# Optimization experiments

Measured on AMD Instinct MI355X. Metric: run time of the kernel, lower is better.

The kernel has to match this reference:

```python
import jax, jax.numpy as jnp
import numpy as np

VOCAB = 50257
HID = 1024
MAXLEN = 64


def setup_inputs() -> dict:
    key = jax.random.key(0)
    ks = jax.random.split(key, 12)
    s = 1.0 / np.sqrt(HID)
    return {
        "input": jax.random.randint(ks[0], (1,), 0, VOCAB),
        "hidden": jax.random.normal(ks[1], (1, 1, HID), jnp.float32),
        "enc_outputs": jax.random.normal(ks[2], (MAXLEN, HID), jnp.float32),
        "emb": jax.random.normal(ks[3], (VOCAB, HID), jnp.float32),
        "attn_W": jax.random.uniform(ks[4], (MAXLEN, 2 * HID), jnp.float32, -s, s),
        "attn_b": jnp.zeros((MAXLEN,), jnp.float32),
        "comb_W": jax.random.uniform(ks[5], (HID, 2 * HID), jnp.float32, -s, s),
        "comb_b": jnp.zeros((HID,), jnp.float32),
        "gru_Wih": jax.random.uniform(ks[6], (3 * HID, HID), jnp.float32, -s, s),
        "gru_Whh": jax.random.uniform(ks[7], (3 * HID, HID), jnp.float32, -s, s),
        "gru_bih": jnp.zeros((3 * HID,), jnp.float32),
        "gru_bhh": jnp.zeros((3 * HID,), jnp.float32),
        "out_W": jax.random.uniform(ks[8], (VOCAB, HID), jnp.float32, -s, s),
        "out_b": jnp.zeros((VOCAB,), jnp.float32),
    }


def reference(input, hidden, enc_outputs, emb, attn_W, attn_b, comb_W, comb_b,
              gru_Wih, gru_Whh, gru_bih, gru_bhh, out_W, out_b):
    # embedded: [1, HID] (dropout is identity in eval / p=0)
    embedded = emb[input[0]][None, :]
    h = hidden[0]  # [1, HID]
    # attention over encoder positions
    cat_eh = jnp.concatenate([embedded, h], axis=1)           # [1, 2H]
    attn_weights = jax.nn.softmax(cat_eh @ attn_W.T + attn_b, axis=1)  # [1, MAXLEN]
    attn_applied = attn_weights @ enc_outputs                  # [1, HID]
    # combine
    x = jnp.concatenate([embedded, attn_applied], axis=1)      # [1, 2H]
    x = jax.nn.relu(x @ comb_W.T + comb_b)                     # [1, HID]
    # single GRU step (PyTorch gate order: r, z, n)
    gi = x @ gru_Wih.T + gru_bih                                # [1, 3H]
    gh = h @ gru_Whh.T + gru_bhh                                # [1, 3H]
    i_r, i_z, i_n = jnp.split(gi, 3, axis=1)
    h_r, h_z, h_n = jnp.split(gh, 3, axis=1)
    r = jax.nn.sigmoid(i_r + h_r)
    z = jax.nn.sigmoid(i_z + h_z)
    n = jnp.tanh(i_n + r * h_n)
    h_new = (1.0 - z) * n + z * h                               # [1, HID]
    # output projection + log-softmax
    logp = jax.nn.log_softmax(h_new @ out_W.T + out_b, axis=1)  # [1, VOCAB]
    return logp, h_new[None, :, :], attn_weights
```

## Files before the change

kernel.cpp:

```cpp
#include <hip/hip_runtime.h>
#include <hip/hip_bf16.h>

#define VOCAB 50257
#define HID   1024
#define MAXLEN 64

__device__ __forceinline__ float dot4(float4 a, float4 b){
  return a.x*b.x + a.y*b.y + a.z*b.z + a.w*b.w;
}
__device__ __forceinline__ float dot4f(float4 a, const float* v){
  return a.x*v[0] + a.y*v[1] + a.z*v[2] + a.w*v[3];
}

__global__ __launch_bounds__(256) void k_attn_scores(
    const int* tok_p, const float* hidden, const float* emb,
    const float* attn_W, const float* attn_b, float* ws_scores){
  int b = blockIdx.x, t = threadIdx.x;
  int tok = min(max(tok_p[0], 0), VOCAB-1);
  const float4* wv = (const float4*)(attn_W + (size_t)b*2048);
  const float4* ef = (const float4*)(emb + (size_t)tok*HID);
  const float4* hf = (const float4*)hidden;
  float acc = dot4(wv[t], ef[t]) + dot4(wv[256+t], hf[t]);
  #pragma unroll
  for (int k=32;k>=1;k>>=1) acc += __shfl_xor(acc,k);
  __shared__ float red[4];
  if ((t&63)==0) red[t>>6] = acc;
  __syncthreads();
  if (t==0) ws_scores[b] = red[0]+red[1]+red[2]+red[3] + attn_b[b];
}

__global__ __launch_bounds__(256) void k_combine_fused(
    const int* tok_p, const float* ws_scores, const float* enc,
    const float* emb, const float* comb_W, const float* comb_b,
    float* ws_x, float* out_attn){
  int t = threadIdx.x, wave = t>>6, lane = t&63;
  __shared__ float sw[MAXLEN];
  __shared__ float sa[HID];
  float s = ws_scores[lane];
  float m = s;
  #pragma unroll
  for (int k=32;k>=1;k>>=1) m = fmaxf(m, __shfl_xor(m,k));
  float e = expf(s-m), d = e;
  #pragma unroll
  for (int k=32;k>=1;k>>=1) d += __shfl_xor(d,k);
  float w = e/d;
  if (wave==0) sw[lane] = w;
  if (blockIdx.x==0 && wave==0) out_attn[lane] = w;
  __syncthreads();
  float4 a4 = make_float4(0.f,0.f,0.f,0.f);
  #pragma unroll 8
  for (int p=0;p<MAXLEN;p++){
    float wp = sw[p];
    float4 ev = *(const float4*)(enc + (size_t)p*HID + t*4);
    a4.x += wp*ev.x; a4.y += wp*ev.y; a4.z += wp*ev.z; a4.w += wp*ev.w;
  }
  *(float4*)(sa + t*4) = a4;
  __syncthreads();
  int row = blockIdx.x*4 + wave;
  int tok = min(max(tok_p[0], 0), VOCAB-1);
  const float4* wrow = (const float4*)(comb_W + (size_t)row*2048);
  const float4* erow = (const float4*)(emb + (size_t)tok*HID);
  const float4* av   = (const float4*)sa;
  float acc = 0.f;
  #pragma unroll
  for (int c=0;c<4;c++) acc += dot4(wrow[c*64+lane],     erow[c*64+lane]);
  #pragma unroll
  for (int c=0;c<4;c++) acc += dot4(wrow[256+c*64+lane], av[c*64+lane]);
  #pragma unroll
  for (int k=32;k>=1;k>>=1) acc += __shfl_xor(acc,k);
  if (lane==0) ws_x[row] = fmaxf(acc + comb_b[row], 0.f);
}

__global__ __launch_bounds__(256) void k_gru_fused(
    const float* ws_x, const float* hidden,
    const float* Wih, const float* Whh,
    const float* bih, const float* bhh,
    float* ws_h, float* out_h){
  int t = threadIdx.x, wave = t>>6, lane = t&63;
  __shared__ float part[2][6];
  for (int idx = wave; idx < 12; idx += 4){
    int u  = (idx >= 6) ? 1 : 0;
    int g  = idx - u*6;
    int hi = blockIdx.x*2 + u;
    bool ih = (g < 3);
    int gg = ih ? g : g-3;
    const float*  W = ih ? Wih : Whh;
    const float*  b = ih ? bih : bhh;
    const float4* vec  = ih ? (const float4*)ws_x : (const float4*)hidden;
    const float4* wrow = (const float4*)(W + ((size_t)gg*HID + hi)*HID);
    float acc = 0.f;
    #pragma unroll
    for (int c=0;c<4;c++) acc += dot4(wrow[c*64+lane], vec[c*64+lane]);
    #pragma unroll
    for (int k=32;k>=1;k>>=1) acc += __shfl_xor(acc,k);
    if (lane==0) part[u][g] = acc + b[gg*HID + hi];
  }
  __syncthreads();
  if (t < 2){
    int hi = blockIdx.x*2 + t;
    float r = 1.f/(1.f+expf(-(part[t][0] + part[t][3])));
    float z = 1.f/(1.f+expf(-(part[t][1] + part[t][4])));
    float n = tanhf(part[t][2] + r*part[t][5]);
    float h = hidden[hi];
    float hn = (1.f-z)*n + z*h;
    ws_h[hi]  = hn;
    out_h[hi] = hn;
  }
}

__global__ __launch_bounds__(256) void k_logits(
    const float* wsh, const float* out_W, const float* out_b,
    float* out_logits, float* ws_stats){
  int wave = threadIdx.x>>6, lane = threadIdx.x&63;
  int gw = blockIdx.x*4 + wave;
  float hv[16];
  #pragma unroll
  for (int c=0;c<4;c++)
    #pragma unroll
    for (int j=0;j<4;j++) hv[c*4+j] = wsh[c*256 + lane*4 + j];
  float m = -INFINITY, s = 0.f;
  for (int row = gw; row < VOCAB; row += 8192) {
    const float4* wrow = (const float4*)(out_W + (size_t)row*HID);
    float acc = 0.f;
    #pragma unroll
    for (int c=0;c<4;c++) acc += dot4f(wrow[c*64+lane], hv + c*4);
    #pragma unroll
    for (int k=32;k>=1;k>>=1) acc += __shfl_xor(acc,k);
    if (lane==0) {
      float logit = acc + out_b[row];
      out_logits[row] = logit;
      if (logit > m) { s = s*expf(m-logit) + 1.f; m = logit; }
      else s += expf(logit-m);
    }
  }
  __shared__ float sm[4], ss[4];
  if (lane==0){ sm[wave]=m; ss[wave]=s; }
  __syncthreads();
  if (threadIdx.x==0) {
    float M = fmaxf(fmaxf(sm[0],sm[1]),fmaxf(sm[2],sm[3]));
    float S = ss[0]*expf(sm[0]-M)+ss[1]*expf(sm[1]-M)
            + ss[2]*expf(sm[2]-M)+ss[3]*expf(sm[3]-M);
    ws_stats[blockIdx.x*2]   = M;
    ws_stats[blockIdx.x*2+1] = S;
  }
}

__global__ __launch_bounds__(256) void k_logp_fused(
    const float* ws_stats, float* out_logits){
  int t = threadIdx.x;
  float m = -INFINITY, s = 0.f;
  #pragma unroll
  for (int i=t;i<2048;i+=256){
    float mi = ws_stats[2*i], si = ws_stats[2*i+1];
    float M = fmaxf(m,mi);
    s = s*expf(m-M) + si*expf(mi-M);
    m = M;
  }
  #pragma unroll
  for (int k=32;k>=1;k>>=1){
    float mo = __shfl_xor(m,k), so = __shfl_xor(s,k);
    float M = fmaxf(m,mo);
    s = s*expf(m-M) + so*expf(mo-M);
    m = M;
  }
  __shared__ float sm[4], ss[4];
  __shared__ float slse;
  if ((t&63)==0){ sm[t>>6]=m; ss[t>>6]=s; }
  __syncthreads();
  if (t==0){
    float M = fmaxf(fmaxf(sm[0],sm[1]),fmaxf(sm[2],sm[3]));
    float S = ss[0]*expf(sm[0]-M)+ss[1]*expf(sm[1]-M)
            + ss[2]*expf(sm[2]-M)+ss[3]*expf(sm[3]-M);
    slse = M + logf(S);
  }
  __syncthreads();
  int i = blockIdx.x*256 + t;
  if (i < VOCAB) out_logits[i] -= slse;
}

extern "C" void kernel_launch(void* const* d_in, const int* in_sizes, int n_in,
                              void* d_out, int out_size, void* d_ws, size_t ws_size,
                              hipStream_t stream) {
  const int*   tok    = (const int*)d_in[0];
  const float* hidden = (const float*)d_in[1];
  const float* enc    = (const float*)d_in[2];
  const float* emb    = (const float*)d_in[3];
  const float* attn_W = (const float*)d_in[4];
  const float* attn_b = (const float*)d_in[5];
  const float* comb_W = (const float*)d_in[6];
  const float* comb_b = (const float*)d_in[7];
  const float* Wih    = (const float*)d_in[8];
  const float* Whh    = (const float*)d_in[9];
  const float* bih    = (const float*)d_in[10];
  const float* bhh    = (const float*)d_in[11];
  const float* out_W  = (const float*)d_in[12];
  const float* out_b  = (const float*)d_in[13];

  float* out      = (float*)d_out;
  float* out_logp = out;
  float* out_h    = out + VOCAB;
  float* out_attn = out + VOCAB + HID;

  float* ws        = (float*)d_ws;
  float* ws_scores = ws;
  float* ws_x      = ws + 128;
  float* ws_h      = ws + 1280;
  float* ws_stats  = ws + 2432;

  k_attn_scores  <<<64,   256, 0, stream>>>(tok, hidden, emb, attn_W, attn_b, ws_scores);
  k_combine_fused<<<256,  256, 0, stream>>>(tok, ws_scores, enc, emb, comb_W, comb_b, ws_x, out_attn);
  k_gru_fused    <<<512,  256, 0, stream>>>(ws_x, hidden, Wih, Whh, bih, bhh, ws_h, out_h);
  k_logits       <<<2048, 256, 0, stream>>>(ws_h, out_W, out_b, out_logp, ws_stats);
  k_logp_fused   <<<197,  256, 0, stream>>>(ws_stats, out_logp);
}
```

Baseline: 422.9 us.

## Fuse attention scores into combine kernel and reshape GRU kernel to one unit per block

Each combine block now computes all 64 attention scores itself, dropping the separate score kernel and one launch. The cost is that 256 blocks each redundantly read the full attn_W (512 KB), though this should mostly be served from cache. The GRU kernel now launches 1024 blocks of 6 waves, one wave per gate row, instead of 512 blocks that each looped over 12 rows. That gives more parallelism and removes the loop.

```diff
diff --git a/kernel.cpp b/kernel.cpp
--- a/kernel.cpp
+++ b/kernel.cpp
@@ -12,31 +12,32 @@
   return a.x*v[0] + a.y*v[1] + a.z*v[2] + a.w*v[3];
 }
 
-__global__ __launch_bounds__(256) void k_attn_scores(
-    const int* tok_p, const float* hidden, const float* emb,
-    const float* attn_W, const float* attn_b, float* ws_scores){
-  int b = blockIdx.x, t = threadIdx.x;
-  int tok = min(max(tok_p[0], 0), VOCAB-1);
-  const float4* wv = (const float4*)(attn_W + (size_t)b*2048);
-  const float4* ef = (const float4*)(emb + (size_t)tok*HID);
-  const float4* hf = (const float4*)hidden;
-  float acc = dot4(wv[t], ef[t]) + dot4(wv[256+t], hf[t]);
-  #pragma unroll
-  for (int k=32;k>=1;k>>=1) acc += __shfl_xor(acc,k);
-  __shared__ float red[4];
-  if ((t&63)==0) red[t>>6] = acc;
-  __syncthreads();
-  if (t==0) ws_scores[b] = red[0]+red[1]+red[2]+red[3] + attn_b[b];
-}
-
 __global__ __launch_bounds__(256) void k_combine_fused(
-    const int* tok_p, const float* ws_scores, const float* enc,
-    const float* emb, const float* comb_W, const float* comb_b,
+    const int* tok_p, const float* hidden, const float* enc,
+    const float* emb, const float* attn_W, const float* attn_b,
+    const float* comb_W, const float* comb_b,
     float* ws_x, float* out_attn){
   int t = threadIdx.x, wave = t>>6, lane = t&63;
   __shared__ float sw[MAXLEN];
   __shared__ float sa[HID];
-  float s = ws_scores[lane];
+  int tok = min(max(tok_p[0], 0), VOCAB-1);
+  const float4* ef = (const float4*)(emb + (size_t)tok*HID);
+  const float4* hf = (const float4*)hidden;
+  #pragma unroll
+  for (int i=0;i<16;i++){
+    int b = wave*16 + i;
+    const float4* wv = (const float4*)(attn_W + (size_t)b*2048);
+    float acc = 0.f;
+    #pragma unroll
+    for (int c=0;c<4;c++) acc += dot4(wv[c*64+lane],     ef[c*64+lane]);
+    #pragma unroll
+    for (int c=0;c<4;c++) acc += dot4(wv[256+c*64+lane], hf[c*64+lane]);
+    #pragma unroll
+    for (int k=32;k>=1;k>>=1) acc += __shfl_xor(acc,k);
+    if (lane==0) sw[b] = acc + attn_b[b];
+  }
+  __syncthreads();
+  float s = sw[lane];
   float m = s;
   #pragma unroll
   for (int k=32;k>=1;k>>=1) m = fmaxf(m, __shfl_xor(m,k));
@@ -44,6 +45,7 @@
   #pragma unroll
   for (int k=32;k>=1;k>>=1) d += __shfl_xor(d,k);
   float w = e/d;
+  __syncthreads();
   if (wave==0) sw[lane] = w;
   if (blockIdx.x==0 && wave==0) out_attn[lane] = w;
   __syncthreads();
@@ -57,13 +59,11 @@
   *(float4*)(sa + t*4) = a4;
   __syncthreads();
   int row = blockIdx.x*4 + wave;
-  int tok = min(max(tok_p[0], 0), VOCAB-1);
   const float4* wrow = (const float4*)(comb_W + (size_t)row*2048);
-  const float4* erow = (const float4*)(emb + (size_t)tok*HID);
   const float4* av   = (const float4*)sa;
   float acc = 0.f;
   #pragma unroll
-  for (int c=0;c<4;c++) acc += dot4(wrow[c*64+lane],     erow[c*64+lane]);
+  for (int c=0;c<4;c++) acc += dot4(wrow[c*64+lane],     ef[c*64+lane]);
   #pragma unroll
   for (int c=0;c<4;c++) acc += dot4(wrow[256+c*64+lane], av[c*64+lane]);
   #pragma unroll
@@ -71,36 +71,31 @@
   if (lane==0) ws_x[row] = fmaxf(acc + comb_b[row], 0.f);
 }
 
-__global__ __launch_bounds__(256) void k_gru_fused(
+__global__ __launch_bounds__(384) void k_gru_fused(
     const float* ws_x, const float* hidden,
     const float* Wih, const float* Whh,
     const float* bih, const float* bhh,
     float* ws_h, float* out_h){
   int t = threadIdx.x, wave = t>>6, lane = t&63;
-  __shared__ float part[2][6];
-  for (int idx = wave; idx < 12; idx += 4){
-    int u  = (idx >= 6) ? 1 : 0;
-    int g  = idx - u*6;
-    int hi = blockIdx.x*2 + u;
-    bool ih = (g < 3);
-    int gg = ih ? g : g-3;
-    const float*  W = ih ? Wih : Whh;
-    const float*  b = ih ? bih : bhh;
-    const float4* vec  = ih ? (const float4*)ws_x : (const float4*)hidden;
-    const float4* wrow = (const float4*)(W + ((size_t)gg*HID + hi)*HID);
-    float acc = 0.f;
-    #pragma unroll
-    for (int c=0;c<4;c++) acc += dot4(wrow[c*64+lane], vec[c*64+lane]);
-    #pragma unroll
-    for (int k=32;k>=1;k>>=1) acc += __shfl_xor(acc,k);
-    if (lane==0) part[u][g] = acc + b[gg*HID + hi];
-  }
-  __syncthreads();
-  if (t < 2){
-    int hi = blockIdx.x*2 + t;
-    float r = 1.f/(1.f+expf(-(part[t][0] + part[t][3])));
-    float z = 1.f/(1.f+expf(-(part[t][1] + part[t][4])));
-    float n = tanhf(part[t][2] + r*part[t][5]);
+  int hi = blockIdx.x;
+  __shared__ float part[6];
+  bool ih = (wave < 3);
+  int gg = ih ? wave : wave-3;
+  const float*  W = ih ? Wih : Whh;
+  const float*  b = ih ? bih : bhh;
+  const float4* vec  = ih ? (const float4*)ws_x : (const float4*)hidden;
+  const float4* wrow = (const float4*)(W + ((size_t)gg*HID + hi)*HID);
+  float acc = 0.f;
+  #pragma unroll
+  for (int c=0;c<4;c++) acc += dot4(wrow[c*64+lane], vec[c*64+lane]);
+  #pragma unroll
+  for (int k=32;k>=1;k>>=1) acc += __shfl_xor(acc,k);
+  if (lane==0) part[wave] = acc + b[gg*HID + hi];
+  __syncthreads();
+  if (t==0){
+    float r = 1.f/(1.f+expf(-(part[0] + part[3])));
+    float z = 1.f/(1.f+expf(-(part[1] + part[4])));
+    float n = tanhf(part[2] + r*part[5]);
     float h = hidden[hi];
     float hn = (1.f-z)*n + z*h;
     ws_h[hi]  = hn;
@@ -202,14 +197,13 @@
   float* out_attn = out + VOCAB + HID;
 
   float* ws        = (float*)d_ws;
-  float* ws_scores = ws;
-  float* ws_x      = ws + 128;
-  float* ws_h      = ws + 1280;
-  float* ws_stats  = ws + 2432;
-
-  k_attn_scores  <<<64,   256, 0, stream>>>(tok, hidden, emb, attn_W, attn_b, ws_scores);
-  k_combine_fused<<<256,  256, 0, stream>>>(tok, ws_scores, enc, emb, comb_W, comb_b, ws_x, out_attn);
-  k_gru_fused    <<<512,  256, 0, stream>>>(ws_x, hidden, Wih, Whh, bih, bhh, ws_h, out_h);
+  float* ws_x      = ws;
+  float* ws_h      = ws + 1024;
+  float* ws_stats  = ws + 2048;
+
+  k_combine_fused<<<256,  256, 0, stream>>>(tok, hidden, enc, emb, attn_W, attn_b,
+                                            comb_W, comb_b, ws_x, out_attn);
+  k_gru_fused    <<<1024, 384, 0, stream>>>(ws_x, hidden, Wih, Whh, bih, bhh, ws_h, out_h);
   k_logits       <<<2048, 256, 0, stream>>>(ws_h, out_W, out_b, out_logp, ws_stats);
   k_logp_fused   <<<197,  256, 0, stream>>>(ws_stats, out_logp);
 }
```

Measured after the change: 431.3 us. No clear change (+2.0%).
